# Kernel optimization log

Hardware: AMD Instinct MI355X
Metric: run time of the kernel (lower is better)

## Reference

```python
import jax, jax.numpy as jnp
import numpy as np

N = 40000   # nodes
E = 600000  # edges
G = 64      # graphs
DIN = 128   # input feature dim
H = 128     # hidden_channels
L = 3       # num_layers


def setup_inputs() -> dict:
    key = jax.random.key(0)
    ks = jax.random.split(key, 16)
    s = 0.05
    inp = {}
    inp["x"] = jax.random.normal(ks[0], (N, DIN), jnp.float32)
    inp["edge_attr"] = jax.random.normal(ks[1], (E,), jnp.float32)
    inp["node_w"] = jax.random.normal(ks[2], (DIN, H), jnp.float32) * s
    inp["node_b"] = jnp.zeros((H,), jnp.float32)
    inp["edge_w"] = jax.random.normal(ks[3], (1, H), jnp.float32) * s
    inp["edge_b"] = jnp.zeros((H,), jnp.float32)
    inp["t"] = jnp.ones((L,), jnp.float32)  # learn_t init 1.0
    inp["lin1_w"] = jax.random.normal(ks[4], (L, H, 2 * H), jnp.float32) * s
    inp["lin1_b"] = jnp.zeros((L, 2 * H), jnp.float32)
    inp["ln1_g"] = jnp.ones((L, 2 * H), jnp.float32)
    inp["ln1_bt"] = jnp.zeros((L, 2 * H), jnp.float32)
    inp["lin2_w"] = jax.random.normal(ks[5], (L, 2 * H, H), jnp.float32) * s
    inp["lin2_b"] = jnp.zeros((L, H), jnp.float32)
    inp["blk_g"] = jnp.ones((L, H), jnp.float32)
    inp["blk_b"] = jnp.zeros((L, H), jnp.float32)
    inp["hw1"] = jax.random.normal(ks[6], (H, H // 2), jnp.float32) * s
    inp["hb1"] = jnp.zeros((H // 2,), jnp.float32)
    inp["hw2"] = jax.random.normal(ks[7], (H // 2, H // 4), jnp.float32) * s
    inp["hb2"] = jnp.zeros((H // 4,), jnp.float32)
    inp["hw3"] = jax.random.normal(ks[8], (H // 4, 1), jnp.float32) * s
    inp["hb3"] = jnp.zeros((1,), jnp.float32)
    inp["edge_index"] = jax.random.randint(ks[9], (2, E), 0, N, jnp.int32)
    inp["batch"] = jnp.sort(jax.random.randint(ks[10], (N,), 0, G, jnp.int32))
    return inp


def _layer_norm(v, g, b):
    mu = jnp.mean(v, axis=-1, keepdims=True)
    var = jnp.var(v, axis=-1, keepdims=True)
    return (v - mu) * jax.lax.rsqrt(var + 1e-5) * g + b


def reference(x, edge_attr, node_w, node_b, edge_w, edge_b, t,
              lin1_w, lin1_b, ln1_g, ln1_bt, lin2_w, lin2_b,
              blk_g, blk_b, hw1, hb1, hw2, hb2, hw3, hb3,
              edge_index, batch):
    src, dst = edge_index[0], edge_index[1]
    h = x @ node_w + node_b                       # [N, H]
    ea = edge_attr[:, None] @ edge_w + edge_b     # [E, H]

    def genconv(xn, i):
        # message: relu(x_j + e) + eps
        msg = jax.nn.relu(xn[src] + ea) + 1e-7    # [E, H]
        # scatter-softmax over dst with learnable temperature t
        logit = msg * t[i]
        m = jax.ops.segment_max(logit, dst, num_segments=N)
        m = jnp.where(jnp.isfinite(m), m, 0.0)    # isolated nodes
        ex = jnp.exp(logit - m[dst])
        den = jax.ops.segment_sum(ex, dst, num_segments=N)
        agg = jax.ops.segment_sum(ex * msg, dst, num_segments=N) / jnp.maximum(den, 1e-16)
        o = agg + xn                              # add root
        # GENConv MLP: Linear(H,2H) -> LayerNorm -> ReLU -> Linear(2H,H)
        o = jax.nn.relu(_layer_norm(o @ lin1_w[i] + lin1_b[i], ln1_g[i], ln1_bt[i]))
        return o @ lin2_w[i] + lin2_b[i]

    # layer 0: bare conv (as in the torch forward)
    h = genconv(h, 0)
    # layers 1..L-1: DeepGCNLayer res+ (norm -> act -> [dropout=id in eval] -> conv -> residual)
    for i in range(1, L):
        r = jax.nn.relu(_layer_norm(h, blk_g[i], blk_b[i]))
        h = h + genconv(r, i)
    # final norm+act uses layer 0's norm/act
    h = jax.nn.relu(_layer_norm(h, blk_g[0], blk_b[0]))
    # global mean pool over graphs
    cnt = jax.ops.segment_sum(jnp.ones((N,), h.dtype), batch, num_segments=G)
    pooled = jax.ops.segment_sum(h, batch, num_segments=G) / jnp.maximum(cnt, 1.0)[:, None]
    # MLP head (dropout = identity in eval)
    o = jax.nn.relu(pooled @ hw1 + hb1)
    o = jax.nn.relu(o @ hw2 + hb2)
    return o @ hw3 + hb3                          # [G, 1]
```

## Files before the change

### kernel.cpp

```cpp
#include <hip/hip_runtime.h>
#include <math.h>

#define NN 40000
#define NE 600000
#define NG 64
#define DIM_IN 128
#define HH 128
#define HH2 256

using half8 = __attribute__((ext_vector_type(8))) _Float16;
using h2    = __attribute__((ext_vector_type(2))) _Float16;
using f4    = __attribute__((ext_vector_type(4))) float;

__device__ __forceinline__ int lower_bound_dev(const int* a, int n, int key) {
    int lo = 0, hi = n;
    while (lo < hi) { int mid = (lo + hi) >> 1; if (a[mid] < key) lo = mid + 1; else hi = mid; }
    return lo;
}

#define NX (NN*DIM_IN)
__global__ void convert_kernel(const float* __restrict__ x, const float* __restrict__ node_w,
                               const float* __restrict__ lin1_w, const float* __restrict__ lin2_w,
                               _Float16* __restrict__ xh, _Float16* __restrict__ nwt,
                               _Float16* __restrict__ w1t, _Float16* __restrict__ w2t)
{
    int id = blockIdx.x * blockDim.x + threadIdx.x;
    if (id < NX) { xh[id] = (_Float16)x[id]; return; }
    id -= NX;
    if (id < 16384) { int n = id >> 7, k = id & 127; nwt[id] = (_Float16)node_w[k*128 + n]; return; }
    id -= 16384;
    if (id < 98304) {
        int l = id >> 15, r = id & 32767;
        int n = r >> 7, k = r & 127;
        w1t[id] = (_Float16)lin1_w[l*32768 + k*256 + n];
        return;
    }
    id -= 98304;
    if (id < 98304) {
        int l = id >> 15, r = id & 32767;
        int n = r >> 8, k = r & 255;
        w2t[id] = (_Float16)lin2_w[l*32768 + k*128 + n];
    }
}

__global__ void count_kernel(const int* __restrict__ dst, int* __restrict__ counts) {
    int e = blockIdx.x * blockDim.x + threadIdx.x;
    if (e < NE) atomicAdd(&counts[dst[e]], 1);
}

__global__ __launch_bounds__(1024) void scan_kernel(const int* __restrict__ counts,
                                                    int* __restrict__ row_ptr,
                                                    int* __restrict__ cursor) {
    __shared__ int wpre[16];
    __shared__ int tot;
    int t = threadIdx.x, lane = t & 63, wid = t >> 6;
    if (t == 0) row_ptr[0] = 0;
    int carry = 0;
    for (int base = 0; base < NN; base += 1024) {
        int i = base + t;
        int v = (i < NN) ? counts[i] : 0;
        int s = v;
        #pragma unroll
        for (int off = 1; off < 64; off <<= 1) {
            int u = __shfl_up(s, off, 64);
            if (lane >= off) s += u;
        }
        if (lane == 63) wpre[wid] = s;
        __syncthreads();
        if (t == 0) {
            int run = 0;
            #pragma unroll
            for (int j = 0; j < 16; ++j) { int xv = wpre[j]; wpre[j] = run; run += xv; }
            tot = run;
        }
        __syncthreads();
        int incl = s + wpre[wid] + carry;
        if (i < NN) { row_ptr[i + 1] = incl; cursor[i] = incl - v; }
        carry += tot;
        __syncthreads();
    }
}

__global__ void fill_kernel(const int* __restrict__ src, const int* __restrict__ dst,
                            const float* __restrict__ eattr, int* __restrict__ cursor,
                            int* __restrict__ src_s, float* __restrict__ attr_s) {
    int e = blockIdx.x * blockDim.x + threadIdx.x;
    if (e < NE) {
        int pos = atomicAdd(&cursor[dst[e]], 1);
        src_s[pos] = src[e];
        attr_s[pos] = eattr[e];
    }
}

__global__ __launch_bounds__(256) void agg_kernel(
    const _Float16* __restrict__ xh,
    const int* __restrict__ row_ptr,
    const int* __restrict__ src_s, const float* __restrict__ attr_s,
    const float* __restrict__ ew, const float* __restrict__ eb,
    const float* __restrict__ tptr, int layer,
    _Float16* __restrict__ oh)
{
    int d = blockIdx.x * 4 + (threadIdx.x >> 6);
    int lane = threadIdx.x & 63;
    int c0 = 2 * lane;
    float tc = tptr[layer];
    float ew0 = ew[c0], eb0 = eb[c0];
    float ew1 = ew[c0 + 1], eb1 = eb[c0 + 1];
    int beg = row_ptr[d], end = row_ptr[d + 1];
    float den0 = 0.f, num0 = 0.f, den1 = 0.f, num1 = 0.f;
    for (int base = beg; base < end; base += 64) {
        int cnt = min(64, end - base);
        int gl = base + min(lane, cnt - 1);
        int sv = src_s[gl];
        float av = attr_s[gl];
        for (int j0 = 0; j0 < cnt; j0 += 8) {
            h2 g[8]; float aa[8];
            #pragma unroll
            for (int u = 0; u < 8; ++u) {
                int jj = min(j0 + u, cnt - 1);
                int s = __shfl(sv, jj, 64);
                aa[u] = __shfl(av, jj, 64);
                g[u] = *(const h2*)(xh + ((size_t)s << 7) + c0);
            }
            int lim = min(8, cnt - j0);
            #pragma unroll
            for (int u = 0; u < 8; ++u) {
                if (u < lim) {
                    float m0 = fmaxf(__fmaf_rn(aa[u], ew0, eb0) + (float)g[u].x, 0.f) + 1e-7f;
                    float m1 = fmaxf(__fmaf_rn(aa[u], ew1, eb1) + (float)g[u].y, 0.f) + 1e-7f;
                    float e0 = __expf(m0 * tc), e1 = __expf(m1 * tc);
                    den0 += e0; num0 = __fmaf_rn(e0, m0, num0);
                    den1 += e1; num1 = __fmaf_rn(e1, m1, num1);
                }
            }
        }
    }
    h2 sv2 = *(const h2*)(xh + ((size_t)d << 7) + c0);
    float o0 = num0 / fmaxf(den0, 1e-16f) + (float)sv2.x;
    float o1 = num1 / fmaxf(den1, 1e-16f) + (float)sv2.y;
    h2 ov; ov.x = (_Float16)o0; ov.y = (_Float16)o1;
    *(h2*)(oh + ((size_t)d << 7) + c0) = ov;
}

__global__ __launch_bounds__(256) void gemm_mfma(
    const _Float16* __restrict__ A, const _Float16* __restrict__ Bt,
    const float* __restrict__ bias, _Float16* __restrict__ C,
    int M, int N, int K)
{
    constexpr int LDA = 40;
    __shared__ _Float16 As[64 * LDA];
    __shared__ _Float16 Bs[128 * LDA];
    int t = threadIdx.x;
    int row0 = blockIdx.y * 64;
    int col0 = blockIdx.x * 128;
    int w = t >> 6, lane = t & 63;
    int wm = w & 1, wn = w >> 1;
    int q = lane >> 4, l16 = lane & 15;
    f4 acc[2][4];
    #pragma unroll
    for (int i = 0; i < 2; ++i)
        #pragma unroll
        for (int j = 0; j < 4; ++j)
            acc[i][j] = (f4){0.f, 0.f, 0.f, 0.f};

    for (int k0 = 0; k0 < K; k0 += 32) {
        {
            int r = t >> 2, seg = t & 3;
            *(float4*)&As[r * LDA + seg * 8] =
                *(const float4*)(A + (size_t)(row0 + r) * K + k0 + seg * 8);
        }
        #pragma unroll
        for (int i = 0; i < 2; ++i) {
            int idx = t + i * 256;
            int r = idx >> 2, seg = idx & 3;
            *(float4*)&Bs[r * LDA + seg * 8] =
                *(const float4*)(Bt + (size_t)(col0 + r) * K + k0 + seg * 8);
        }
        __syncthreads();
        half8 af[2], bf[4];
        #pragma unroll
        for (int i = 0; i < 2; ++i)
            af[i] = *(const half8*)&As[(wm * 32 + i * 16 + l16) * LDA + q * 8];
        #pragma unroll
        for (int j = 0; j < 4; ++j)
            bf[j] = *(const half8*)&Bs[(wn * 64 + j * 16 + l16) * LDA + q * 8];
        #pragma unroll
        for (int i = 0; i < 2; ++i)
            #pragma unroll
            for (int j = 0; j < 4; ++j)
                acc[i][j] = __builtin_amdgcn_mfma_f32_16x16x32_f16(af[i], bf[j], acc[i][j], 0, 0, 0);
        __syncthreads();
    }
    #pragma unroll
    for (int j = 0; j < 4; ++j) {
        int col = col0 + wn * 64 + j * 16 + l16;
        float bv = bias[col];
        #pragma unroll
        for (int i = 0; i < 2; ++i) {
            int rbase = row0 + wm * 32 + i * 16 + q * 4;
            #pragma unroll
            for (int rg = 0; rg < 4; ++rg)
                C[(size_t)(rbase + rg) * N + col] = (_Float16)(acc[i][j][rg] + bv);
        }
    }
}

template<int RES>
__global__ __launch_bounds__(256) void mlp_fused(
    const _Float16* __restrict__ Ain,
    const _Float16* __restrict__ w1t,
    const float* __restrict__ b1,
    const float* __restrict__ g1, const float* __restrict__ bt1,
    const _Float16* __restrict__ w2t,
    const float* __restrict__ b2,
    float* __restrict__ h,
    const float* __restrict__ bg, const float* __restrict__ bb,
    _Float16* __restrict__ xout)
{
    constexpr int LDA = 136;
    constexpr int LDB = 40;
    constexpr int LDM = 264;
    __shared__ _Float16 As[64 * LDA];
    __shared__ _Float16 Bs[256 * LDB];
    __shared__ _Float16 midh[64 * LDM];
    __shared__ float ssum[64][2], ssum2[64][2];
    int t = threadIdx.x;
    int row0 = blockIdx.x * 64;
    int w = t >> 6, lane = t & 63;
    int wm = w & 1, wn = w >> 1;
    int q = lane >> 4, l16 = lane & 15;

    #pragma unroll
    for (int p = 0; p < 4; ++p) {
        int idx = t + p * 256;
        int r = idx >> 4, seg = idx & 15;
        *(float4*)&As[r * LDA + seg * 8] =
            *(const float4*)(Ain + (size_t)(row0 + r) * 128 + seg * 8);
    }

    f4 acc[2][8];
    #pragma unroll
    for (int i = 0; i < 2; ++i)
        #pragma unroll
        for (int j = 0; j < 8; ++j)
            acc[i][j] = (f4){0.f, 0.f, 0.f, 0.f};
    for (int k0 = 0; k0 < 128; k0 += 32) {
        #pragma unroll
        for (int p = 0; p < 4; ++p) {
            int idx = t + p * 256;
            int r = idx >> 2, seg = idx & 3;
            *(float4*)&Bs[r * LDB + seg * 8] =
                *(const float4*)(w1t + (size_t)r * 128 + k0 + seg * 8);
        }
        __syncthreads();
        half8 af[2], bf[8];
        #pragma unroll
        for (int i = 0; i < 2; ++i)
            af[i] = *(const half8*)&As[(wm * 32 + i * 16 + l16) * LDA + k0 + q * 8];
        #pragma unroll
        for (int j = 0; j < 8; ++j)
            bf[j] = *(const half8*)&Bs[(wn * 128 + j * 16 + l16) * LDB + q * 8];
        #pragma unroll
        for (int i = 0; i < 2; ++i)
            #pragma unroll
            for (int j = 0; j < 8; ++j)
                acc[i][j] = __builtin_amdgcn_mfma_f32_16x16x32_f16(af[i], bf[j], acc[i][j], 0, 0, 0);
        __syncthreads();
    }

    float b1v[8], g1v[8], bt1v[8];
    #pragma unroll
    for (int j = 0; j < 8; ++j) {
        int col = wn * 128 + j * 16 + l16;
        b1v[j] = b1[col]; g1v[j] = g1[col]; bt1v[j] = bt1[col];
    }
    float vals[2][8][4];
    #pragma unroll
    for (int i = 0; i < 2; ++i)
        #pragma unroll
        for (int j = 0; j < 8; ++j)
            #pragma unroll
            for (int rg = 0; rg < 4; ++rg)
                vals[i][j][rg] = acc[i][j][rg] + b1v[j];
    #pragma unroll
    for (int i = 0; i < 2; ++i) {
        #pragma unroll
        for (int rg = 0; rg < 4; ++rg) {
            float ps = 0.f, ps2 = 0.f;
            #pragma unroll
            for (int j = 0; j < 8; ++j) { float v = vals[i][j][rg]; ps += v; ps2 += v * v; }
            #pragma unroll
            for (int off = 1; off < 16; off <<= 1) {
                ps  += __shfl_xor(ps,  off, 16);
                ps2 += __shfl_xor(ps2, off, 16);
            }
            if (l16 == 0) {
                int row = wm * 32 + i * 16 + q * 4 + rg;
                ssum[row][wn] = ps; ssum2[row][wn] = ps2;
            }
        }
    }
    __syncthreads();
    #pragma unroll
    for (int i = 0; i < 2; ++i) {
        #pragma unroll
        for (int rg = 0; rg < 4; ++rg) {
            int row = wm * 32 + i * 16 + q * 4 + rg;
            float S = ssum[row][0] + ssum[row][1];
            float S2 = ssum2[row][0] + ssum2[row][1];
            float mu = S * (1.0f / 256.0f);
            float var = S2 * (1.0f / 256.0f) - mu * mu;
            float rstd = rsqrtf(var + 1e-5f);
            #pragma unroll
            for (int j = 0; j < 8; ++j) {
                int col = wn * 128 + j * 16 + l16;
                float o = fmaxf((vals[i][j][rg] - mu) * rstd * g1v[j] + bt1v[j], 0.f);
                midh[row * LDM + col] = (_Float16)o;
            }
        }
    }
    __syncthreads();

    f4 acc2[2][4];
    #pragma unroll
    for (int i = 0; i < 2; ++i)
        #pragma unroll
        for (int j = 0; j < 4; ++j)
            acc2[i][j] = (f4){0.f, 0.f, 0.f, 0.f};
    for (int k0 = 0; k0 < 256; k0 += 32) {
        #pragma unroll
        for (int p = 0; p < 2; ++p) {
            int idx = t + p * 256;
            int r = idx >> 2, seg = idx & 3;
            *(float4*)&Bs[r * LDB + seg * 8] =
                *(const float4*)(w2t + (size_t)r * 256 + k0 + seg * 8);
        }
        __syncthreads();
        half8 af2[2], bf2[4];
        #pragma unroll
        for (int i = 0; i < 2; ++i)
            af2[i] = *(const half8*)&midh[(wm * 32 + i * 16 + l16) * LDM + k0 + q * 8];
        #pragma unroll
        for (int j = 0; j < 4; ++j)
            bf2[j] = *(const half8*)&Bs[(wn * 64 + j * 16 + l16) * LDB + q * 8];
        #pragma unroll
        for (int i = 0; i < 2; ++i)
            #pragma unroll
            for (int j = 0; j < 4; ++j)
                acc2[i][j] = __builtin_amdgcn_mfma_f32_16x16x32_f16(af2[i], bf2[j], acc2[i][j], 0, 0, 0);
        __syncthreads();
    }

    float b2v[4], bgv[4], bbv[4];
    #pragma unroll
    for (int j = 0; j < 4; ++j) {
        int col = wn * 64 + j * 16 + l16;
        b2v[j] = b2[col]; bgv[j] = bg[col]; bbv[j] = bb[col];
    }
    float ov[2][4][4];
    #pragma unroll
    for (int i = 0; i < 2; ++i) {
        #pragma unroll
        for (int rg = 0; rg < 4; ++rg) {
            int row = wm * 32 + i * 16 + q * 4 + rg;
            #pragma unroll
            for (int j = 0; j < 4; ++j) {
                int col = wn * 64 + j * 16 + l16;
                float v = acc2[i][j][rg] + b2v[j];
                size_t gidx = (size_t)(row0 + row) * 128 + col;
                if (RES) v += h[gidx];
                h[gidx] = v;
                ov[i][j][rg] = v;
            }
        }
    }
    #pragma unroll
    for (int i = 0; i < 2; ++i) {
        #pragma unroll
        for (int rg = 0; rg < 4; ++rg) {
            float ps = 0.f, ps2 = 0.f;
            #pragma unroll
            for (int j = 0; j < 4; ++j) { float v = ov[i][j][rg]; ps += v; ps2 += v * v; }
            #pragma unroll
            for (int off = 1; off < 16; off <<= 1) {
                ps  += __shfl_xor(ps,  off, 16);
                ps2 += __shfl_xor(ps2, off, 16);
            }
            if (l16 == 0) {
                int row = wm * 32 + i * 16 + q * 4 + rg;
                ssum[row][wn] = ps; ssum2[row][wn] = ps2;
            }
        }
    }
    __syncthreads();
    #pragma unroll
    for (int i = 0; i < 2; ++i) {
        #pragma unroll
        for (int rg = 0; rg < 4; ++rg) {
            int row = wm * 32 + i * 16 + q * 4 + rg;
            float S = ssum[row][0] + ssum[row][1];
            float S2 = ssum2[row][0] + ssum2[row][1];
            float mu = S * (1.0f / 128.0f);
            float var = S2 * (1.0f / 128.0f) - mu * mu;
            float rstd = rsqrtf(var + 1e-5f);
            #pragma unroll
            for (int j = 0; j < 4; ++j) {
                int col = wn * 64 + j * 16 + l16;
                float o = fmaxf((ov[i][j][rg] - mu) * rstd * bgv[j] + bbv[j], 0.f);
                xout[(size_t)(row0 + row) * 128 + col] = (_Float16)o;
            }
        }
    }
}

__global__ __launch_bounds__(128) void pool_kernel(
    const _Float16* __restrict__ f, const int* __restrict__ batch, float* __restrict__ pooled)
{
    int g = blockIdx.x;
    int chunk = blockIdx.y;
    int c = threadIdx.x;
    int s = lower_bound_dev(batch, NN, g);
    int e = lower_bound_dev(batch, NN, g + 1);
    int len = e - s;
    if (len <= 0) return;
    int nch = gridDim.y;
    int per = (len + nch - 1) / nch;
    int cs = s + chunk * per;
    int ce = min(cs + per, e);
    if (cs >= ce) return;
    float acc = 0.f;
    for (int n = cs; n < ce; ++n) acc += (float)f[(size_t)n * HH + c];
    atomicAdd(&pooled[g * HH + c], acc);
}

__global__ __launch_bounds__(128) void head_kernel(
    const float* __restrict__ pooled, const int* __restrict__ batch,
    const float* __restrict__ hw1, const float* __restrict__ hb1,
    const float* __restrict__ hw2, const float* __restrict__ hb2,
    const float* __restrict__ hw3, const float* __restrict__ hb3,
    float* __restrict__ out)
{
    __shared__ float p[HH];
    __shared__ float o1[64];
    __shared__ float o2[32];
    int g = blockIdx.x;
    int t = threadIdx.x;
    int s = lower_bound_dev(batch, NN, g);
    int e = lower_bound_dev(batch, NN, g + 1);
    float cnt = fmaxf((float)(e - s), 1.0f);
    p[t] = pooled[g * HH + t] / cnt;
    __syncthreads();
    if (t < 64) {
        float acc = hb1[t];
        for (int k = 0; k < HH; ++k) acc += p[k] * hw1[k * 64 + t];
        o1[t] = fmaxf(acc, 0.f);
    }
    __syncthreads();
    if (t < 32) {
        float acc = hb2[t];
        for (int k = 0; k < 64; ++k) acc += o1[k] * hw2[k * 32 + t];
        o2[t] = fmaxf(acc, 0.f);
    }
    __syncthreads();
    if (t == 0) {
        float acc = hb3[0];
        for (int k = 0; k < 32; ++k) acc += o2[k] * hw3[k];
        out[g] = acc;
    }
}

extern "C" void kernel_launch(void* const* d_in, const int* in_sizes, int n_in,
                              void* d_out, int out_size, void* d_ws, size_t ws_size,
                              hipStream_t stream)
{
    const float* x      = (const float*)d_in[0];
    const float* eattr  = (const float*)d_in[1];
    const float* node_w = (const float*)d_in[2];
    const float* node_b = (const float*)d_in[3];
    const float* edge_w = (const float*)d_in[4];
    const float* edge_b = (const float*)d_in[5];
    const float* tptr   = (const float*)d_in[6];
    const float* lin1_w = (const float*)d_in[7];
    const float* lin1_b = (const float*)d_in[8];
    const float* ln1_g  = (const float*)d_in[9];
    const float* ln1_bt = (const float*)d_in[10];
    const float* lin2_w = (const float*)d_in[11];
    const float* lin2_b = (const float*)d_in[12];
    const float* blk_g  = (const float*)d_in[13];
    const float* blk_b  = (const float*)d_in[14];
    const float* hw1    = (const float*)d_in[15];
    const float* hb1    = (const float*)d_in[16];
    const float* hw2    = (const float*)d_in[17];
    const float* hb2    = (const float*)d_in[18];
    const float* hw3    = (const float*)d_in[19];
    const float* hb3    = (const float*)d_in[20];
    const int*   eidx   = (const int*)d_in[21];
    const int*   batch  = (const int*)d_in[22];
    const int* src = eidx;
    const int* dst = eidx + NE;
    float* out = (float*)d_out;

    char* ws = (char*)d_ws;
    size_t off = 0;
    auto carve = [&](size_t bytes) -> char* {
        char* p = ws + off;
        off = (off + bytes + 255) & ~(size_t)255;
        return p;
    };
    float*    h      = (float*)carve((size_t)NN * HH * 4);
    _Float16* xh_in  = (_Float16*)carve((size_t)NX * 2);
    _Float16* xnh    = (_Float16*)carve((size_t)NN * HH * 2);
    _Float16* oh     = (_Float16*)carve((size_t)NN * HH * 2);
    _Float16* rh     = (_Float16*)carve((size_t)NN * HH * 2);
    _Float16* nwt    = (_Float16*)carve((size_t)16384 * 2);
    _Float16* w1t    = (_Float16*)carve((size_t)98304 * 2);
    _Float16* w2t    = (_Float16*)carve((size_t)98304 * 2);
    int*      counts = (int*)carve((size_t)NN * 4);
    int*      rowp   = (int*)carve((size_t)(NN + 1) * 4);
    int*      cursor = (int*)carve((size_t)NN * 4);
    int*      src_s  = (int*)carve((size_t)NE * 4);
    float*    attr_s = (float*)carve((size_t)NE * 4);
    float*    pooled = (float*)carve((size_t)NG * HH * 4);

    hipMemsetAsync(counts, 0, (size_t)NN * 4, stream);
    hipMemsetAsync(pooled, 0, (size_t)NG * HH * 4, stream);

    {
        int total = NX + 16384 + 98304 + 98304;
        convert_kernel<<<(total + 255) / 256, 256, 0, stream>>>(
            x, node_w, lin1_w, lin2_w, xh_in, nwt, w1t, w2t);
    }
    count_kernel<<<(NE + 255) / 256, 256, 0, stream>>>(dst, counts);
    scan_kernel<<<1, 1024, 0, stream>>>(counts, rowp, cursor);
    fill_kernel<<<(NE + 255) / 256, 256, 0, stream>>>(src, dst, eattr, cursor, src_s, attr_s);

    gemm_mfma<<<dim3(1, NN / 64), 256, 0, stream>>>(xh_in, nwt, node_b, xnh, NN, HH, DIM_IN);

    agg_kernel<<<NN / 4, 256, 0, stream>>>(xnh, rowp, src_s, attr_s, edge_w, edge_b, tptr, 0, oh);
    mlp_fused<0><<<NN / 64, 256, 0, stream>>>(
        oh, w1t, lin1_b, ln1_g, ln1_bt, w2t, lin2_b,
        h, blk_g + 1 * HH, blk_b + 1 * HH, xnh);
    agg_kernel<<<NN / 4, 256, 0, stream>>>(xnh, rowp, src_s, attr_s, edge_w, edge_b, tptr, 1, oh);
    mlp_fused<1><<<NN / 64, 256, 0, stream>>>(
        oh, w1t + 32768, lin1_b + HH2, ln1_g + HH2, ln1_bt + HH2, w2t + 32768, lin2_b + HH,
        h, blk_g + 2 * HH, blk_b + 2 * HH, xnh);
    agg_kernel<<<NN / 4, 256, 0, stream>>>(xnh, rowp, src_s, attr_s, edge_w, edge_b, tptr, 2, oh);
    mlp_fused<1><<<NN / 64, 256, 0, stream>>>(
        oh, w1t + 2 * 32768, lin1_b + 2 * HH2, ln1_g + 2 * HH2, ln1_bt + 2 * HH2,
        w2t + 2 * 32768, lin2_b + 2 * HH,
        h, blk_g, blk_b, rh);

    pool_kernel<<<dim3(NG, 8), 128, 0, stream>>>(rh, batch, pooled);
    head_kernel<<<NG, 128, 0, stream>>>(pooled, batch, hw1, hb1, hw2, hb2, hw3, hb3, out);
}
```

Before: 457.3 us.

## Parallelize CSR build, pack edge records, double-buffer gather loads, vectorize convert

Several independent changes land together. The single-block serial scan becomes a three-kernel multi-block scan. Edge ranks are captured during counting, so the fill step needs no second atomic pass. Source index and edge attribute are packed into one int2 record so each edge needs a single load. The aggregation loop double-buffers its gathers, issuing the next 8 neighbour loads before consuming the current 8 to hide latency, and the x-to-fp16 conversion is vectorized to float4. The cost is extra workspace, more kernel launches and higher register pressure in the aggregation kernel.

```diff
diff --git a/kernel.cpp b/kernel.cpp
--- a/kernel.cpp
+++ b/kernel.cpp
@@ -9,6 +9,7 @@
 #define HH2 256
 
 using half8 = __attribute__((ext_vector_type(8))) _Float16;
+using half4 = __attribute__((ext_vector_type(4))) _Float16;
 using h2    = __attribute__((ext_vector_type(2))) _Float16;
 using f4    = __attribute__((ext_vector_type(4))) float;
 
@@ -19,14 +20,20 @@
 }
 
 #define NX (NN*DIM_IN)
+#define NX4 (NX/4)
 __global__ void convert_kernel(const float* __restrict__ x, const float* __restrict__ node_w,
                                const float* __restrict__ lin1_w, const float* __restrict__ lin2_w,
                                _Float16* __restrict__ xh, _Float16* __restrict__ nwt,
                                _Float16* __restrict__ w1t, _Float16* __restrict__ w2t)
 {
     int id = blockIdx.x * blockDim.x + threadIdx.x;
-    if (id < NX) { xh[id] = (_Float16)x[id]; return; }
-    id -= NX;
+    if (id < NX4) {
+        float4 v = *(const float4*)(x + (size_t)id * 4);
+        half4 o; o.x = (_Float16)v.x; o.y = (_Float16)v.y; o.z = (_Float16)v.z; o.w = (_Float16)v.w;
+        *(half4*)(xh + (size_t)id * 4) = o;
+        return;
+    }
+    id -= NX4;
     if (id < 16384) { int n = id >> 7, k = id & 127; nwt[id] = (_Float16)node_w[k*128 + n]; return; }
     id -= 16384;
     if (id < 98304) {
@@ -43,59 +50,71 @@
     }
 }
 
-__global__ void count_kernel(const int* __restrict__ dst, int* __restrict__ counts) {
+__global__ void count_rank_kernel(const int* __restrict__ dst, int* __restrict__ counts,
+                                  int* __restrict__ rank) {
     int e = blockIdx.x * blockDim.x + threadIdx.x;
-    if (e < NE) atomicAdd(&counts[dst[e]], 1);
-}
-
-__global__ __launch_bounds__(1024) void scan_kernel(const int* __restrict__ counts,
-                                                    int* __restrict__ row_ptr,
-                                                    int* __restrict__ cursor) {
+    if (e < NE) rank[e] = atomicAdd(&counts[dst[e]], 1);
+}
+
+__global__ __launch_bounds__(1024) void scanA_kernel(const int* __restrict__ counts,
+                                                     int* __restrict__ tmp, int* __restrict__ btot) {
     __shared__ int wpre[16];
-    __shared__ int tot;
     int t = threadIdx.x, lane = t & 63, wid = t >> 6;
-    if (t == 0) row_ptr[0] = 0;
-    int carry = 0;
-    for (int base = 0; base < NN; base += 1024) {
-        int i = base + t;
-        int v = (i < NN) ? counts[i] : 0;
-        int s = v;
-        #pragma unroll
-        for (int off = 1; off < 64; off <<= 1) {
-            int u = __shfl_up(s, off, 64);
-            if (lane >= off) s += u;
-        }
-        if (lane == 63) wpre[wid] = s;
-        __syncthreads();
-        if (t == 0) {
-            int run = 0;
-            #pragma unroll
-            for (int j = 0; j < 16; ++j) { int xv = wpre[j]; wpre[j] = run; run += xv; }
-            tot = run;
-        }
-        __syncthreads();
-        int incl = s + wpre[wid] + carry;
-        if (i < NN) { row_ptr[i + 1] = incl; cursor[i] = incl - v; }
-        carry += tot;
-        __syncthreads();
-    }
-}
-
-__global__ void fill_kernel(const int* __restrict__ src, const int* __restrict__ dst,
-                            const float* __restrict__ eattr, int* __restrict__ cursor,
-                            int* __restrict__ src_s, float* __restrict__ attr_s) {
+    int i = blockIdx.x * 1024 + t;
+    int v = (i < NN) ? counts[i] : 0;
+    int s = v;
+    #pragma unroll
+    for (int off = 1; off < 64; off <<= 1) {
+        int u = __shfl_up(s, off, 64);
+        if (lane >= off) s += u;
+    }
+    if (lane == 63) wpre[wid] = s;
+    __syncthreads();
+    if (t == 0) {
+        int run = 0;
+        #pragma unroll
+        for (int j = 0; j < 16; ++j) { int xv = wpre[j]; wpre[j] = run; run += xv; }
+        btot[blockIdx.x] = run;
+    }
+    __syncthreads();
+    if (i < NN) tmp[i] = s + wpre[wid];
+}
+
+__global__ __launch_bounds__(64) void scanB_kernel(const int* __restrict__ btot,
+                                                   int* __restrict__ boff, int nb) {
+    int t = threadIdx.x;
+    int v = (t < nb) ? btot[t] : 0;
+    int s = v;
+    #pragma unroll
+    for (int off = 1; off < 64; off <<= 1) {
+        int u = __shfl_up(s, off, 64);
+        if (t >= off) s += u;
+    }
+    if (t < nb) boff[t] = s - v;
+}
+
+__global__ __launch_bounds__(1024) void scanC_kernel(const int* __restrict__ tmp,
+                                                     const int* __restrict__ boff,
+                                                     int* __restrict__ rowp) {
+    int i = blockIdx.x * 1024 + threadIdx.x;
+    if (i < NN) rowp[i + 1] = tmp[i] + boff[blockIdx.x];
+    if (i == 0) rowp[0] = 0;
+}
+
+__global__ void fill2_kernel(const int* __restrict__ src, const int* __restrict__ dst,
+                             const float* __restrict__ eattr, const int* __restrict__ rowp,
+                             const int* __restrict__ rank, int2* __restrict__ rec) {
     int e = blockIdx.x * blockDim.x + threadIdx.x;
     if (e < NE) {
-        int pos = atomicAdd(&cursor[dst[e]], 1);
-        src_s[pos] = src[e];
-        attr_s[pos] = eattr[e];
+        int pos = rowp[dst[e]] + rank[e];
+        rec[pos] = make_int2(src[e], __float_as_int(eattr[e]));
     }
 }
 
 __global__ __launch_bounds__(256) void agg_kernel(
     const _Float16* __restrict__ xh,
     const int* __restrict__ row_ptr,
-    const int* __restrict__ src_s, const float* __restrict__ attr_s,
+    const int2* __restrict__ rec,
     const float* __restrict__ ew, const float* __restrict__ eb,
     const float* __restrict__ tptr, int layer,
     _Float16* __restrict__ oh)
@@ -110,11 +129,11 @@
     float den0 = 0.f, num0 = 0.f, den1 = 0.f, num1 = 0.f;
     for (int base = beg; base < end; base += 64) {
         int cnt = min(64, end - base);
-        int gl = base + min(lane, cnt - 1);
-        int sv = src_s[gl];
-        float av = attr_s[gl];
-        for (int j0 = 0; j0 < cnt; j0 += 8) {
-            h2 g[8]; float aa[8];
+        int2 mv = rec[base + min(lane, cnt - 1)];
+        int sv = mv.x;
+        float av = __int_as_float(mv.y);
+        h2 gA[8], gB[8]; float aA[8], aB[8];
+        auto issue = [&](h2 (&g)[8], float (&aa)[8], int j0) {
             #pragma unroll
             for (int u = 0; u < 8; ++u) {
                 int jj = min(j0 + u, cnt - 1);
@@ -122,6 +141,8 @@
                 aa[u] = __shfl(av, jj, 64);
                 g[u] = *(const h2*)(xh + ((size_t)s << 7) + c0);
             }
+        };
+        auto consume = [&](h2 (&g)[8], float (&aa)[8], int j0) {
             int lim = min(8, cnt - j0);
             #pragma unroll
             for (int u = 0; u < 8; ++u) {
@@ -133,6 +154,13 @@
                     den1 += e1; num1 = __fmaf_rn(e1, m1, num1);
                 }
             }
+        };
+        issue(gA, aA, 0);
+        for (int j0 = 0; j0 < cnt; j0 += 16) {
+            if (j0 + 8 < cnt)  issue(gB, aB, j0 + 8);
+            consume(gA, aA, j0);
+            if (j0 + 16 < cnt) issue(gA, aA, j0 + 16);
+            if (j0 + 8 < cnt)  consume(gB, aB, j0 + 8);
         }
     }
     h2 sv2 = *(const h2*)(xh + ((size_t)d << 7) + c0);
@@ -516,35 +544,40 @@
     _Float16* w1t    = (_Float16*)carve((size_t)98304 * 2);
     _Float16* w2t    = (_Float16*)carve((size_t)98304 * 2);
     int*      counts = (int*)carve((size_t)NN * 4);
+    int*      rank   = (int*)carve((size_t)NE * 4);
+    int*      tmp    = (int*)carve((size_t)NN * 4);
+    int*      btot   = (int*)carve((size_t)64 * 4);
+    int*      boff   = (int*)carve((size_t)64 * 4);
     int*      rowp   = (int*)carve((size_t)(NN + 1) * 4);
-    int*      cursor = (int*)carve((size_t)NN * 4);
-    int*      src_s  = (int*)carve((size_t)NE * 4);
-    float*    attr_s = (float*)carve((size_t)NE * 4);
+    int2*     rec    = (int2*)carve((size_t)NE * 8);
     float*    pooled = (float*)carve((size_t)NG * HH * 4);
 
     hipMemsetAsync(counts, 0, (size_t)NN * 4, stream);
     hipMemsetAsync(pooled, 0, (size_t)NG * HH * 4, stream);
 
     {
-        int total = NX + 16384 + 98304 + 98304;
+        int total = NX4 + 16384 + 98304 + 98304;
         convert_kernel<<<(total + 255) / 256, 256, 0, stream>>>(
             x, node_w, lin1_w, lin2_w, xh_in, nwt, w1t, w2t);
     }
-    count_kernel<<<(NE + 255) / 256, 256, 0, stream>>>(dst, counts);
-    scan_kernel<<<1, 1024, 0, stream>>>(counts, rowp, cursor);
-    fill_kernel<<<(NE + 255) / 256, 256, 0, stream>>>(src, dst, eattr, cursor, src_s, attr_s);
+    const int NB = (NN + 1023) / 1024;
+    count_rank_kernel<<<(NE + 255) / 256, 256, 0, stream>>>(dst, counts, rank);
+    scanA_kernel<<<NB, 1024, 0, stream>>>(counts, tmp, btot);
+    scanB_kernel<<<1, 64, 0, stream>>>(btot, boff, NB);
+    scanC_kernel<<<NB, 1024, 0, stream>>>(tmp, boff, rowp);
+    fill2_kernel<<<(NE + 255) / 256, 256, 0, stream>>>(src, dst, eattr, rowp, rank, rec);
 
     gemm_mfma<<<dim3(1, NN / 64), 256, 0, stream>>>(xh_in, nwt, node_b, xnh, NN, HH, DIM_IN);
 
-    agg_kernel<<<NN / 4, 256, 0, stream>>>(xnh, rowp, src_s, attr_s, edge_w, edge_b, tptr, 0, oh);
+    agg_kernel<<<NN / 4, 256, 0, stream>>>(xnh, rowp, rec, edge_w, edge_b, tptr, 0, oh);
     mlp_fused<0><<<NN / 64, 256, 0, stream>>>(
         oh, w1t, lin1_b, ln1_g, ln1_bt, w2t, lin2_b,
         h, blk_g + 1 * HH, blk_b + 1 * HH, xnh);
-    agg_kernel<<<NN / 4, 256, 0, stream>>>(xnh, rowp, src_s, attr_s, edge_w, edge_b, tptr, 1, oh);
+    agg_kernel<<<NN / 4, 256, 0, stream>>>(xnh, rowp, rec, edge_w, edge_b, tptr, 1, oh);
     mlp_fused<1><<<NN / 64, 256, 0, stream>>>(
         oh, w1t + 32768, lin1_b + HH2, ln1_g + HH2, ln1_bt + HH2, w2t + 32768, lin2_b + HH,
         h, blk_g + 2 * HH, blk_b + 2 * HH, xnh);
-    agg_kernel<<<NN / 4, 256, 0, stream>>>(xnh, rowp, src_s, attr_s, edge_w, edge_b, tptr, 2, oh);
+    agg_kernel<<<NN / 4, 256, 0, stream>>>(xnh, rowp, rec, edge_w, edge_b, tptr, 2, oh);
     mlp_fused<1><<<NN / 64, 256, 0, stream>>>(
         oh, w1t + 2 * 32768, lin1_b + 2 * HH2, ln1_g + 2 * HH2, ln1_bt + 2 * HH2,
         w2t + 2 * 32768, lin2_b + 2 * HH,
```

Result: faster. 394.0 us (-13.8%).
